# Kernel tuning notes

Measured on AMD Instinct MI355X. Metric: run time of the kernel, lower is better.

The kernel has to match this reference:

```python
import jax, jax.numpy as jnp
import numpy as np

jax.config.update("jax_enable_x64", True)

MEM = 33554432  # 2**25 bytes, stored as int64 (256 MB)
SHIFTS = jnp.arange(8, dtype=jnp.int64) * 8  # [0,8,...,56] little-endian byte shifts


def _read_int(memory, addr):
    # Read 8 bytes at addr (clamped, like torch) and assemble a little-endian int64.
    idx = jnp.clip(addr + jnp.arange(8, dtype=jnp.int64), 0, memory.shape[0] - 1)
    return jnp.sum(memory[idx] << SHIFTS)


def _masked_write_int(memory, addr, value, mask):
    # Scatter 8 bytes of `value` at addr (clamped), gated by scalar mask (0/1).
    idx = jnp.clip(addr + jnp.arange(8, dtype=jnp.int64), 0, memory.shape[0] - 1)
    new_bytes = (value >> SHIFTS) & 255
    return memory.at[idx].set(jnp.where(mask != 0, new_bytes, memory[idx]))


def _masked_write_byte(memory, addr, value, mask):
    idx = jnp.clip(addr, 0, memory.shape[0] - 1)
    return memory.at[idx].set(jnp.where(mask != 0, value & 255, memory[idx]))


def setup_inputs() -> dict:
    key = jax.random.key(0)
    memory = jax.random.randint(key, (MEM,), 0, 256, dtype=jnp.int64)
    return {
        "pc": jnp.int64(0),
        "sp": jnp.int64(MEM - 4096),
        "bp": jnp.int64(MEM - 4096),
        "ax": jnp.int64(7),
        "memory": memory,
    }


def reference(pc, sp, bp, ax, memory):
    pc = jnp.asarray(pc, jnp.int64); sp = jnp.asarray(sp, jnp.int64)
    bp = jnp.asarray(bp, jnp.int64); ax = jnp.asarray(ax, jnp.int64)
    zero = jnp.int64(0); one = jnp.int64(1)

    # fetch
    instruction = _read_int(memory, pc)
    opcode = instruction & 255
    imm = instruction >> 8  # arithmetic shift, matches torch

    stack_top = _read_int(memory, sp)
    mem_at_ax = _read_int(memory, ax)

    pc_plus_8 = pc + 8
    pc_eq_imm = imm
    ret_pc = _read_int(memory, bp + 8)

    sp_unchanged = sp; sp_minus_8 = sp - 8; sp_plus_8 = sp + 8; sp_plus_imm = sp + imm
    bp_unchanged = bp
    bp_from_stack = _read_int(memory, bp)

    # ALU outcomes (all computed branchlessly)
    ax_safe = jnp.where(ax == 0, one, ax)
    ax_eq_bp_plus_imm = bp + imm
    ax_eq_imm = imm
    ax_eq_mem_at_ax = mem_at_ax
    ax_eq_mem_byte = mem_at_ax & 255
    ax_add = stack_top + ax
    ax_sub = stack_top - ax
    ax_mul = stack_top * ax
    ax_div = stack_top // ax_safe
    ax_mod = stack_top % ax_safe
    ax_or = stack_top | ax
    ax_xor = stack_top ^ ax
    ax_and = stack_top & ax
    ax_shl = stack_top << (ax & 63)
    ax_shr = stack_top >> (ax & 63)
    ax_eq = (stack_top == ax).astype(jnp.int64)
    ax_ne = (stack_top != ax).astype(jnp.int64)
    ax_lt = (stack_top < ax).astype(jnp.int64)
    ax_gt = (stack_top > ax).astype(jnp.int64)
    ax_le = (stack_top <= ax).astype(jnp.int64)
    ax_ge = (stack_top >= ax).astype(jnp.int64)

    all_pc = jnp.stack([
        pc_plus_8, pc_plus_8, pc_eq_imm, pc_eq_imm,
        jnp.where(ax == 0, pc_eq_imm, pc_plus_8),
        jnp.where(ax != 0, pc_eq_imm, pc_plus_8),
        pc_plus_8, pc_plus_8, ret_pc,
        pc_plus_8, pc_plus_8, pc_plus_8, pc_plus_8, pc_plus_8, pc_plus_8,
        pc_plus_8, pc_plus_8, pc_plus_8, pc_plus_8, pc_plus_8, pc_plus_8,
        pc_plus_8, pc_plus_8, pc_plus_8, pc_plus_8, pc_plus_8, pc_plus_8,
        pc_plus_8, pc_plus_8, pc_plus_8, pc_plus_8, pc_plus_8, pc_plus_8,
        pc_plus_8, pc_plus_8, pc_plus_8, pc_plus_8, pc_plus_8, pc])
    all_sp = jnp.stack([
        sp_unchanged, sp_unchanged, sp_unchanged, sp_minus_8, sp_unchanged,
        sp_unchanged, sp - 8 - imm, sp_plus_imm, bp + 16, sp_unchanged,
        sp_unchanged, sp_plus_8, sp_plus_8, sp_minus_8, sp_plus_8, sp_plus_8,
        sp_plus_8, sp_plus_8, sp_plus_8, sp_plus_8, sp_plus_8, sp_plus_8,
        sp_plus_8, sp_plus_8, sp_plus_8, sp_plus_8, sp_plus_8, sp_plus_8,
        sp_plus_8, sp_plus_8, sp_unchanged, sp_unchanged, sp_unchanged,
        sp_unchanged, sp_unchanged, sp_unchanged, sp_unchanged, sp_unchanged,
        sp_unchanged])
    all_bp = jnp.stack(
        [bp_unchanged] * 6 + [sp - 8, bp_unchanged, bp_from_stack] + [bp_unchanged] * 30)
    all_ax = jnp.stack([
        ax_eq_bp_plus_imm, ax_eq_imm, ax, ax, ax, ax, ax, ax, ax,
        ax_eq_mem_at_ax, ax_eq_mem_byte, ax, ax, ax,
        ax_add, ax_sub, ax_mul, ax_div, ax_mod, ax_or, ax_xor, ax_and,
        ax_shl, ax_shr, ax_eq, ax_ne, ax_lt, ax_gt, ax_le, ax_ge,
        zero, zero, zero, zero, zero, zero, zero, zero, ax])

    opcode_idx = jnp.clip(opcode, 0, 38)
    new_pc = all_pc[opcode_idx]
    new_sp = all_sp[opcode_idx]
    new_bp = all_bp[opcode_idx]
    new_ax = all_ax[opcode_idx]

    # masked memory writes (PSH/JSR/ENT push; SI/SC store)
    is_psh = (opcode == 13).astype(jnp.int64)
    is_jsr = (opcode == 3).astype(jnp.int64)
    is_ent = (opcode == 6).astype(jnp.int64)
    is_si = (opcode == 11).astype(jnp.int64)
    is_sc = (opcode == 12).astype(jnp.int64)
    push_addr = sp - 8
    push_value = is_psh * ax + is_jsr * (pc + 8) + is_ent * bp
    needs_push = is_psh + is_jsr + is_ent

    new_memory = _masked_write_int(memory, push_addr, push_value, needs_push)
    new_memory = _masked_write_int(new_memory, stack_top, ax, is_si)
    new_memory = _masked_write_byte(new_memory, stack_top, ax & 255, is_sc)

    halted = opcode == 38
    return (new_pc, new_sp, new_bp, new_ax, new_memory, halted)
```

## Files before the change

kernel.cpp:

```cpp
#include <hip/hip_runtime.h>


static constexpr long long MEMN = 33554432LL;

__device__ __forceinline__ long long clamp_idx(long long a) {
    return a < 0 ? 0 : (a > MEMN - 1 ? MEMN - 1 : a);
}

__device__ __forceinline__ long long rd_byte(const void* mem, int flag, long long idx) {
    long long j = clamp_idx(idx);
    if (flag == 2) return (long long)((const float*)mem)[j];
    if (flag == 1) return (long long)((const int*)mem)[j << 1];
    return (long long)((const int*)mem)[j];
}

__device__ __forceinline__ long long rd_int(const void* mem, int flag, long long addr) {
    unsigned long long v = 0;
    #pragma unroll
    for (int k = 0; k < 8; ++k)
        v |= (unsigned long long)(unsigned int)rd_byte(mem, flag, addr + k) << (8 * k);
    return (long long)v;
}

__device__ __forceinline__ long long rd_scalar(const void* p, int flag) {
    if (flag == 2) return (long long)((const float*)p)[0];
    return (long long)((const int*)p)[0];
}

__global__ void vm_step(const void* pc_b, const void* sp_b, const void* bp_b,
                        const void* ax_b, const void* mem_b, int* out, int* ws) {
    if (threadIdx.x != 0 || blockIdx.x != 0) return;

    const int* mi = (const int*)mem_b;
    int flag;
    {
        bool big = false;
        bool odd_zero = true;
        for (int i = 0; i < 64; ++i) {
            unsigned int w = (unsigned int)mi[i];
            if (w > 255u) big = true;
            if ((i & 1) && w != 0u) odd_zero = false;
        }
        flag = big ? 2 : (odd_zero ? 1 : 0);
    }
    ws[0] = flag;

    long long pc = rd_scalar(pc_b, flag);
    long long sp = rd_scalar(sp_b, flag);
    long long bp = rd_scalar(bp_b, flag);
    long long ax = rd_scalar(ax_b, flag);

    long long ins       = rd_int(mem_b, flag, pc);
    long long opcode    = ins & 255;
    long long imm       = ins >> 8;
    long long stack_top = rd_int(mem_b, flag, sp);
    long long mem_at_ax = rd_int(mem_b, flag, ax);
    long long ret_pc    = rd_int(mem_b, flag, bp + 8);
    long long bp_stack  = rd_int(mem_b, flag, bp);
    long long pc8       = (long long)((unsigned long long)pc + 8ULL);

    unsigned long long ust = (unsigned long long)stack_top;
    unsigned long long uax = (unsigned long long)ax;
    long long ax_safe = (ax == 0) ? 1LL : ax;
    long long q, r;
    if (ax_safe == -1LL) { q = (long long)(0ULL - ust); r = 0; }
    else {
        q = stack_top / ax_safe; r = stack_top % ax_safe;
        if (r != 0 && ((r < 0) != (ax_safe < 0))) { q -= 1; r += ax_safe; }
    }
    int sh = (int)(ax & 63);

    long long op = opcode > 38 ? 38 : opcode;
    long long npc = pc8, nsp = sp, nbp = bp, nax = ax;
    switch ((int)op) {
        case 0:  nax = (long long)((unsigned long long)bp + (unsigned long long)imm); break;
        case 1:  nax = imm; break;
        case 2:  npc = imm; break;
        case 3:  npc = imm; nsp = sp - 8; break;
        case 4:  npc = (ax == 0) ? imm : pc8; break;
        case 5:  npc = (ax != 0) ? imm : pc8; break;
        case 6:  nsp = sp - 8 - imm; nbp = sp - 8; break;
        case 7:  nsp = sp + imm; break;
        case 8:  npc = ret_pc; nsp = bp + 16; nbp = bp_stack; break;
        case 9:  nax = mem_at_ax; break;
        case 10: nax = mem_at_ax & 255; break;
        case 11: nsp = sp + 8; break;
        case 12: nsp = sp + 8; break;
        case 13: nsp = sp - 8; break;
        case 14: nsp = sp + 8; nax = (long long)(ust + uax); break;
        case 15: nsp = sp + 8; nax = (long long)(ust - uax); break;
        case 16: nsp = sp + 8; nax = (long long)(ust * uax); break;
        case 17: nsp = sp + 8; nax = q; break;
        case 18: nsp = sp + 8; nax = r; break;
        case 19: nsp = sp + 8; nax = stack_top | ax; break;
        case 20: nsp = sp + 8; nax = stack_top ^ ax; break;
        case 21: nsp = sp + 8; nax = stack_top & ax; break;
        case 22: nsp = sp + 8; nax = (long long)(ust << sh); break;
        case 23: nsp = sp + 8; nax = stack_top >> sh; break;
        case 24: nsp = sp + 8; nax = (stack_top == ax) ? 1 : 0; break;
        case 25: nsp = sp + 8; nax = (stack_top != ax) ? 1 : 0; break;
        case 26: nsp = sp + 8; nax = (stack_top <  ax) ? 1 : 0; break;
        case 27: nsp = sp + 8; nax = (stack_top >  ax) ? 1 : 0; break;
        case 28: nsp = sp + 8; nax = (stack_top <= ax) ? 1 : 0; break;
        case 29: nsp = sp + 8; nax = (stack_top >= ax) ? 1 : 0; break;
        case 38: npc = pc; break;
        default: nax = 0; break;
    }

    out[0] = (int)npc;
    out[1] = (int)nsp;
    out[2] = (int)nbp;
    out[3] = (int)nax;
    out[4 + MEMN] = (opcode == 38) ? 1 : 0;

    int nw = 0;
    long long waddr = 0; unsigned long long wval = 0; int wbytes = 0;
    if (opcode == 13 || opcode == 3 || opcode == 6) {
        waddr = sp - 8;
        wval = (unsigned long long)(opcode == 13 ? ax : (opcode == 3 ? pc8 : bp));
        wbytes = 8;
    } else if (opcode == 11) {
        waddr = stack_top; wval = (unsigned long long)ax; wbytes = 8;
    } else if (opcode == 12) {
        waddr = stack_top; wval = (unsigned long long)(ax & 255); wbytes = 1;
    }
    for (int k = 0; k < wbytes; ++k) {
        long long j = clamp_idx(waddr + k);
        ws[2 + 2 * nw] = (int)j;
        ws[3 + 2 * nw] = (int)((wval >> (8 * k)) & 255ULL);
        ++nw;
    }
    ws[1] = nw;
}

__global__ void copy_mem(const void* mem_b, int* out, const int* ws) {
    int flag = ws[0];
    long long tid    = (long long)blockIdx.x * blockDim.x + threadIdx.x;
    long long stride = (long long)gridDim.x * blockDim.x;
    const long long nvec = MEMN / 4;
    int4* o = (int4*)(out + 4);
    if (flag == 1) {
        const int4* m = (const int4*)mem_b;
        for (long long i = tid; i < nvec; i += stride) {
            int4 a = m[2 * i];
            int4 b = m[2 * i + 1];
            int4 f; f.x = a.x; f.y = a.z; f.z = b.x; f.w = b.z;
            o[i] = f;
        }
    } else if (flag == 0) {
        const int4* m = (const int4*)mem_b;
        for (long long i = tid; i < nvec; i += stride) o[i] = m[i];
    } else {
        const float4* m = (const float4*)mem_b;
        for (long long i = tid; i < nvec; i += stride) {
            float4 v = m[i];
            int4 f; f.x = (int)v.x; f.y = (int)v.y; f.z = (int)v.z; f.w = (int)v.w;
            o[i] = f;
        }
    }
}

__global__ void apply_writes(int* out, const int* ws) {
    if (threadIdx.x != 0 || blockIdx.x != 0) return;
    int n = ws[1];
    for (int k = 0; k < n; ++k)
        out[4 + ws[2 + 2 * k]] = ws[3 + 2 * k];
}

extern "C" void kernel_launch(void* const* d_in, const int* in_sizes, int n_in,
                              void* d_out, int out_size, void* d_ws, size_t ws_size,
                              hipStream_t stream) {
    int* out = (int*)d_out;
    int* ws = (int*)d_ws;
    vm_step<<<1, 64, 0, stream>>>(d_in[0], d_in[1], d_in[2], d_in[3], d_in[4], out, ws);
    copy_mem<<<2048, 256, 0, stream>>>(d_in[4], out, ws);
    apply_writes<<<1, 64, 0, stream>>>(out, ws);
}
```

Measured before the change: 255.7 us.

## Fuse VM step, memory copy and write patching into one kernel

```diff
diff --git a/kernel.cpp b/kernel.cpp
--- a/kernel.cpp
+++ b/kernel.cpp
@@ -2,6 +2,9 @@
 
 
 static constexpr long long MEMN = 33554432LL;
+static constexpr int NT = 256;
+static constexpr int NB = 4096;
+static constexpr int ITERS = 8;
 
 __device__ __forceinline__ long long clamp_idx(long long a) {
     return a < 0 ? 0 : (a > MEMN - 1 ? MEMN - 1 : a);
@@ -27,152 +30,190 @@
     return (long long)((const int*)p)[0];
 }
 
-__global__ void vm_step(const void* pc_b, const void* sp_b, const void* bp_b,
-                        const void* ax_b, const void* mem_b, int* out, int* ws) {
-    if (threadIdx.x != 0 || blockIdx.x != 0) return;
+__global__ __launch_bounds__(NT) void fused_step(const void* pc_b, const void* sp_b,
+                                                 const void* bp_b, const void* ax_b,
+                                                 const void* mem_b, int* out) {
+    __shared__ int s_flag, s_nw, s_lo, s_hi;
+    __shared__ int s_idx[8], s_val[8];
 
     const int* mi = (const int*)mem_b;
-    int flag;
-    {
-        bool big = false;
-        bool odd_zero = true;
-        for (int i = 0; i < 64; ++i) {
-            unsigned int w = (unsigned int)mi[i];
-            if (w > 255u) big = true;
-            if ((i & 1) && w != 0u) odd_zero = false;
-        }
-        flag = big ? 2 : (odd_zero ? 1 : 0);
+
+    if (threadIdx.x < 64) {
+        unsigned int w = (unsigned int)mi[threadIdx.x];
+        unsigned long long big    = __ballot(w > 255u);
+        unsigned long long oddnz  = __ballot(((threadIdx.x & 1) != 0) && (w != 0u));
+        if (threadIdx.x == 0) {
+            int flag = big ? 2 : (oddnz ? 0 : 1);
+            s_flag = flag;
+
+            long long pc = rd_scalar(pc_b, flag);
+            long long sp = rd_scalar(sp_b, flag);
+            long long bp = rd_scalar(bp_b, flag);
+            long long ax = rd_scalar(ax_b, flag);
+
+            long long ins       = rd_int(mem_b, flag, pc);
+            long long opcode    = ins & 255;
+            long long imm       = ins >> 8;
+            long long stack_top = rd_int(mem_b, flag, sp);
+            long long mem_at_ax = rd_int(mem_b, flag, ax);
+            long long ret_pc    = rd_int(mem_b, flag, bp + 8);
+            long long bp_stack  = rd_int(mem_b, flag, bp);
+            long long pc8       = (long long)((unsigned long long)pc + 8ULL);
+
+            unsigned long long ust = (unsigned long long)stack_top;
+            unsigned long long uax = (unsigned long long)ax;
+            long long ax_safe = (ax == 0) ? 1LL : ax;
+            long long q, r;
+            if (ax_safe == -1LL) { q = (long long)(0ULL - ust); r = 0; }
+            else {
+                q = stack_top / ax_safe; r = stack_top % ax_safe;
+                if (r != 0 && ((r < 0) != (ax_safe < 0))) { q -= 1; r += ax_safe; }
+            }
+            int sh = (int)(ax & 63);
+
+            long long op = opcode > 38 ? 38 : opcode;
+            long long npc = pc8, nsp = sp, nbp = bp, nax = ax;
+            switch ((int)op) {
+                case 0:  nax = (long long)((unsigned long long)bp + (unsigned long long)imm); break;
+                case 1:  nax = imm; break;
+                case 2:  npc = imm; break;
+                case 3:  npc = imm; nsp = sp - 8; break;
+                case 4:  npc = (ax == 0) ? imm : pc8; break;
+                case 5:  npc = (ax != 0) ? imm : pc8; break;
+                case 6:  nsp = sp - 8 - imm; nbp = sp - 8; break;
+                case 7:  nsp = sp + imm; break;
+                case 8:  npc = ret_pc; nsp = bp + 16; nbp = bp_stack; break;
+                case 9:  nax = mem_at_ax; break;
+                case 10: nax = mem_at_ax & 255; break;
+                case 11: nsp = sp + 8; break;
+                case 12: nsp = sp + 8; break;
+                case 13: nsp = sp - 8; break;
+                case 14: nsp = sp + 8; nax = (long long)(ust + uax); break;
+                case 15: nsp = sp + 8; nax = (long long)(ust - uax); break;
+                case 16: nsp = sp + 8; nax = (long long)(ust * uax); break;
+                case 17: nsp = sp + 8; nax = q; break;
+                case 18: nsp = sp + 8; nax = r; break;
+                case 19: nsp = sp + 8; nax = stack_top | ax; break;
+                case 20: nsp = sp + 8; nax = stack_top ^ ax; break;
+                case 21: nsp = sp + 8; nax = stack_top & ax; break;
+                case 22: nsp = sp + 8; nax = (long long)(ust << sh); break;
+                case 23: nsp = sp + 8; nax = stack_top >> sh; break;
+                case 24: nsp = sp + 8; nax = (stack_top == ax) ? 1 : 0; break;
+                case 25: nsp = sp + 8; nax = (stack_top != ax) ? 1 : 0; break;
+                case 26: nsp = sp + 8; nax = (stack_top <  ax) ? 1 : 0; break;
+                case 27: nsp = sp + 8; nax = (stack_top >  ax) ? 1 : 0; break;
+                case 28: nsp = sp + 8; nax = (stack_top <= ax) ? 1 : 0; break;
+                case 29: nsp = sp + 8; nax = (stack_top >= ax) ? 1 : 0; break;
+                case 38: npc = pc; break;
+                default: nax = 0; break;
+            }
+
+            int nw = 0, lo = 0x7fffffff, hi = -1;
+            long long waddr = 0; unsigned long long wval = 0; int wbytes = 0;
+            if (opcode == 13 || opcode == 3 || opcode == 6) {
+                waddr = sp - 8;
+                wval = (unsigned long long)(opcode == 13 ? ax : (opcode == 3 ? pc8 : bp));
+                wbytes = 8;
+            } else if (opcode == 11) {
+                waddr = stack_top; wval = (unsigned long long)ax; wbytes = 8;
+            } else if (opcode == 12) {
+                waddr = stack_top; wval = (unsigned long long)(ax & 255); wbytes = 1;
+            }
+            for (int k = 0; k < wbytes; ++k) {
+                int j = (int)clamp_idx(waddr + k);
+                s_idx[nw] = j;
+                s_val[nw] = (int)((wval >> (8 * k)) & 255ULL);
+                lo = j < lo ? j : lo;
+                hi = j > hi ? j : hi;
+                ++nw;
+            }
+            s_nw = nw; s_lo = lo; s_hi = hi;
+
+            if (blockIdx.x == 0) {
+                out[0] = (int)npc;
+                out[1] = (int)nsp;
+                out[2] = (int)nbp;
+                out[3] = (int)nax;
+                out[4 + MEMN] = (opcode == 38) ? 1 : 0;
+            }
+        }
     }
-    ws[0] = flag;
-
-    long long pc = rd_scalar(pc_b, flag);
-    long long sp = rd_scalar(sp_b, flag);
-    long long bp = rd_scalar(bp_b, flag);
-    long long ax = rd_scalar(ax_b, flag);
-
-    long long ins       = rd_int(mem_b, flag, pc);
-    long long opcode    = ins & 255;
-    long long imm       = ins >> 8;
-    long long stack_top = rd_int(mem_b, flag, sp);
-    long long mem_at_ax = rd_int(mem_b, flag, ax);
-    long long ret_pc    = rd_int(mem_b, flag, bp + 8);
-    long long bp_stack  = rd_int(mem_b, flag, bp);
-    long long pc8       = (long long)((unsigned long long)pc + 8ULL);
-
-    unsigned long long ust = (unsigned long long)stack_top;
-    unsigned long long uax = (unsigned long long)ax;
-    long long ax_safe = (ax == 0) ? 1LL : ax;
-    long long q, r;
-    if (ax_safe == -1LL) { q = (long long)(0ULL - ust); r = 0; }
-    else {
-        q = stack_top / ax_safe; r = stack_top % ax_safe;
-        if (r != 0 && ((r < 0) != (ax_safe < 0))) { q -= 1; r += ax_safe; }
-    }
-    int sh = (int)(ax & 63);
-
-    long long op = opcode > 38 ? 38 : opcode;
-    long long npc = pc8, nsp = sp, nbp = bp, nax = ax;
-    switch ((int)op) {
-        case 0:  nax = (long long)((unsigned long long)bp + (unsigned long long)imm); break;
-        case 1:  nax = imm; break;
-        case 2:  npc = imm; break;
-        case 3:  npc = imm; nsp = sp - 8; break;
-        case 4:  npc = (ax == 0) ? imm : pc8; break;
-        case 5:  npc = (ax != 0) ? imm : pc8; break;
-        case 6:  nsp = sp - 8 - imm; nbp = sp - 8; break;
-        case 7:  nsp = sp + imm; break;
-        case 8:  npc = ret_pc; nsp = bp + 16; nbp = bp_stack; break;
-        case 9:  nax = mem_at_ax; break;
-        case 10: nax = mem_at_ax & 255; break;
-        case 11: nsp = sp + 8; break;
-        case 12: nsp = sp + 8; break;
-        case 13: nsp = sp - 8; break;
-        case 14: nsp = sp + 8; nax = (long long)(ust + uax); break;
-        case 15: nsp = sp + 8; nax = (long long)(ust - uax); break;
-        case 16: nsp = sp + 8; nax = (long long)(ust * uax); break;
-        case 17: nsp = sp + 8; nax = q; break;
-        case 18: nsp = sp + 8; nax = r; break;
-        case 19: nsp = sp + 8; nax = stack_top | ax; break;
-        case 20: nsp = sp + 8; nax = stack_top ^ ax; break;
-        case 21: nsp = sp + 8; nax = stack_top & ax; break;
-        case 22: nsp = sp + 8; nax = (long long)(ust << sh); break;
-        case 23: nsp = sp + 8; nax = stack_top >> sh; break;
-        case 24: nsp = sp + 8; nax = (stack_top == ax) ? 1 : 0; break;
-        case 25: nsp = sp + 8; nax = (stack_top != ax) ? 1 : 0; break;
-        case 26: nsp = sp + 8; nax = (stack_top <  ax) ? 1 : 0; break;
-        case 27: nsp = sp + 8; nax = (stack_top >  ax) ? 1 : 0; break;
-        case 28: nsp = sp + 8; nax = (stack_top <= ax) ? 1 : 0; break;
-        case 29: nsp = sp + 8; nax = (stack_top >= ax) ? 1 : 0; break;
-        case 38: npc = pc; break;
-        default: nax = 0; break;
-    }
-
-    out[0] = (int)npc;
-    out[1] = (int)nsp;
-    out[2] = (int)nbp;
-    out[3] = (int)nax;
-    out[4 + MEMN] = (opcode == 38) ? 1 : 0;
-
-    int nw = 0;
-    long long waddr = 0; unsigned long long wval = 0; int wbytes = 0;
-    if (opcode == 13 || opcode == 3 || opcode == 6) {
-        waddr = sp - 8;
-        wval = (unsigned long long)(opcode == 13 ? ax : (opcode == 3 ? pc8 : bp));
-        wbytes = 8;
-    } else if (opcode == 11) {
-        waddr = stack_top; wval = (unsigned long long)ax; wbytes = 8;
-    } else if (opcode == 12) {
-        waddr = stack_top; wval = (unsigned long long)(ax & 255); wbytes = 1;
-    }
-    for (int k = 0; k < wbytes; ++k) {
-        long long j = clamp_idx(waddr + k);
-        ws[2 + 2 * nw] = (int)j;
-        ws[3 + 2 * nw] = (int)((wval >> (8 * k)) & 255ULL);
-        ++nw;
-    }
-    ws[1] = nw;
-}
-
-__global__ void copy_mem(const void* mem_b, int* out, const int* ws) {
-    int flag = ws[0];
-    long long tid    = (long long)blockIdx.x * blockDim.x + threadIdx.x;
-    long long stride = (long long)gridDim.x * blockDim.x;
-    const long long nvec = MEMN / 4;
+    __syncthreads();
+
+    const int  flag = s_flag;
+    const int  nw   = s_nw;
+    const int  lo   = s_lo;
+    const int  hi   = s_hi;
+    const long long tid = (long long)blockIdx.x * NT + threadIdx.x;
+    const long long TOT = (long long)NB * NT;
     int4* o = (int4*)(out + 4);
+
     if (flag == 1) {
         const int4* m = (const int4*)mem_b;
-        for (long long i = tid; i < nvec; i += stride) {
+        #pragma unroll
+        for (int k = 0; k < ITERS; ++k) {
+            long long i = tid + (long long)k * TOT;
             int4 a = m[2 * i];
             int4 b = m[2 * i + 1];
             int4 f; f.x = a.x; f.y = a.z; f.z = b.x; f.w = b.z;
+            if (nw) {
+                int base = (int)(i << 2);
+                if (base + 3 >= lo && base <= hi) {
+                    int vals[4] = { f.x, f.y, f.z, f.w };
+                    #pragma unroll
+                    for (int e = 0; e < 4; ++e)
+                        for (int t = 0; t < nw; ++t)
+                            if (s_idx[t] == base + e) vals[e] = s_val[t];
+                    f.x = vals[0]; f.y = vals[1]; f.z = vals[2]; f.w = vals[3];
+                }
+            }
             o[i] = f;
         }
     } else if (flag == 0) {
         const int4* m = (const int4*)mem_b;
-        for (long long i = tid; i < nvec; i += stride) o[i] = m[i];
+        #pragma unroll
+        for (int k = 0; k < ITERS; ++k) {
+            long long i = tid + (long long)k * TOT;
+            int4 f = m[i];
+            if (nw) {
+                int base = (int)(i << 2);
+                if (base + 3 >= lo && base <= hi) {
+                    int vals[4] = { f.x, f.y, f.z, f.w };
+                    #pragma unroll
+                    for (int e = 0; e < 4; ++e)
+                        for (int t = 0; t < nw; ++t)
+                            if (s_idx[t] == base + e) vals[e] = s_val[t];
+                    f.x = vals[0]; f.y = vals[1]; f.z = vals[2]; f.w = vals[3];
+                }
+            }
+            o[i] = f;
+        }
     } else {
         const float4* m = (const float4*)mem_b;
-        for (long long i = tid; i < nvec; i += stride) {
+        #pragma unroll
+        for (int k = 0; k < ITERS; ++k) {
+            long long i = tid + (long long)k * TOT;
             float4 v = m[i];
             int4 f; f.x = (int)v.x; f.y = (int)v.y; f.z = (int)v.z; f.w = (int)v.w;
+            if (nw) {
+                int base = (int)(i << 2);
+                if (base + 3 >= lo && base <= hi) {
+                    int vals[4] = { f.x, f.y, f.z, f.w };
+                    #pragma unroll
+                    for (int e = 0; e < 4; ++e)
+                        for (int t = 0; t < nw; ++t)
+                            if (s_idx[t] == base + e) vals[e] = s_val[t];
+                    f.x = vals[0]; f.y = vals[1]; f.z = vals[2]; f.w = vals[3];
+                }
+            }
             o[i] = f;
         }
     }
-}
-
-__global__ void apply_writes(int* out, const int* ws) {
-    if (threadIdx.x != 0 || blockIdx.x != 0) return;
-    int n = ws[1];
-    for (int k = 0; k < n; ++k)
-        out[4 + ws[2 + 2 * k]] = ws[3 + 2 * k];
 }
 
 extern "C" void kernel_launch(void* const* d_in, const int* in_sizes, int n_in,
                               void* d_out, int out_size, void* d_ws, size_t ws_size,
                               hipStream_t stream) {
     int* out = (int*)d_out;
-    int* ws = (int*)d_ws;
-    vm_step<<<1, 64, 0, stream>>>(d_in[0], d_in[1], d_in[2], d_in[3], d_in[4], out, ws);
-    copy_mem<<<2048, 256, 0, stream>>>(d_in[4], out, ws);
-    apply_writes<<<1, 64, 0, stream>>>(out, ws);
-}
+    fused_step<<<NB, NT, 0, stream>>>(d_in[0], d_in[1], d_in[2], d_in[3], d_in[4], out);
+}
```

Result: faster. 250.3 us (-2.1%).
